# Kernel tuning notes

Hardware: AMD Instinct MI355X
Metric: run time of the kernel (lower is better)

Reference implementation:

```python
import jax, jax.numpy as jnp
import numpy as np

K = 2          # diffusion steps
HID = 64       # hidden_dim
T_OUT = 12     # decoder horizon
EPS = 1e-6


def _random_walk(A):
    # W_fwd = D_out^{-1} A ; W_bwd = D_in^{-1} A^T  (row-normalized)
    W_fwd = A / (A.sum(axis=1, keepdims=True) + EPS)
    AT = A.T
    W_bwd = AT / (AT.sum(axis=1, keepdims=True) + EPS)
    return W_fwd, W_bwd


def _dconv(xin, Wf, Wb, W, b):
    # xin: (B, N, F). K forward + K backward random-walk hops, concat, linear.
    outs = [xin]
    xf = xin
    for _ in range(K):
        xf = jnp.einsum('ij,bjf->bif', Wf, xf)
        outs.append(xf)
    xb = xin
    for _ in range(K):
        xb = jnp.einsum('ij,bjf->bif', Wb, xb)
        outs.append(xb)
    return jnp.concatenate(outs, axis=-1) @ W + b


def _cell(xl, h, Wr, br, Wz, bz, Wn, bn, Wf, Wb):
    xh = jnp.concatenate([xl, h], axis=-1)
    r = jax.nn.sigmoid(_dconv(xh, Wf, Wb, Wr, br))
    z = jax.nn.sigmoid(_dconv(xh, Wf, Wb, Wz, bz))
    xrh = jnp.concatenate([xl, r * h], axis=-1)
    n = jnp.tanh(_dconv(xrh, Wf, Wb, Wn, bn))
    return (1.0 - z) * h + z * n


def setup_inputs() -> dict:
    key = jax.random.key(0)
    ks = jax.random.split(key, 20)
    B, T_in, N = 16, 12, 512
    x = jax.random.normal(ks[0], (B, T_in, N), dtype=jnp.float32)
    A = jax.random.uniform(ks[1], (N, N), dtype=jnp.float32)

    def lin(k, fan_in, fan_out):
        s = 1.0 / np.sqrt(fan_in)
        kw, kb = jax.random.split(k)
        W = jax.random.uniform(kw, (fan_in, fan_out), jnp.float32, -s, s)
        b = jax.random.uniform(kb, (fan_out,), jnp.float32, -s, s)
        return W, b

    in0 = (2 * K + 1) * (1 + HID)    # 325
    in1 = (2 * K + 1) * (2 * HID)    # 640
    Wr0, br0 = lin(ks[2], in0, HID)
    Wz0, bz0 = lin(ks[3], in0, HID)
    Wn0, bn0 = lin(ks[4], in0, HID)
    Wr1, br1 = lin(ks[5], in1, HID)
    Wz1, bz1 = lin(ks[6], in1, HID)
    Wn1, bn1 = lin(ks[7], in1, HID)
    Wp, bp = lin(ks[8], HID, 1)
    return dict(x=x, A=A, Wr0=Wr0, br0=br0, Wz0=Wz0, bz0=bz0, Wn0=Wn0, bn0=bn0,
                Wr1=Wr1, br1=br1, Wz1=Wz1, bz1=bz1, Wn1=Wn1, bn1=bn1, Wp=Wp, bp=bp)


def reference(x, A, Wr0, br0, Wz0, bz0, Wn0, bn0,
              Wr1, br1, Wz1, bz1, Wn1, bn1, Wp, bp):
    Wf, Wb = _random_walk(A)
    B, T_in, N = x.shape
    x4 = x[..., None]                             # (B, T_in, N, 1)
    h0 = jnp.zeros((B, N, HID), x.dtype)
    h1 = jnp.zeros((B, N, HID), x.dtype)

    def enc_step(carry, xt):
        h0, h1 = carry
        h0 = _cell(xt, h0, Wr0, br0, Wz0, bz0, Wn0, bn0, Wf, Wb)
        h1 = _cell(h0, h1, Wr1, br1, Wz1, bz1, Wn1, bn1, Wf, Wb)
        return (h0, h1), None

    (h0, h1), _ = jax.lax.scan(enc_step, (h0, h1), jnp.moveaxis(x4, 1, 0))

    def dec_step(carry, _):
        h0, h1, di = carry
        h0 = _cell(di, h0, Wr0, br0, Wz0, bz0, Wn0, bn0, Wf, Wb)
        h1 = _cell(h0, h1, Wr1, br1, Wz1, bz1, Wn1, bn1, Wf, Wb)
        yt = h1 @ Wp + bp                          # (B, N, 1)
        return (h0, h1, yt), yt

    (_, _, _), ys = jax.lax.scan(dec_step, (h0, h1, x4[:, -1]), None, length=T_OUT)
    return jnp.moveaxis(ys, 0, 1)[..., 0]          # (B, T_out, N)
```

## Files before the change

### kernel.cpp

```cpp
#include <hip/hip_runtime.h>
#include <math.h>

#define T_IN   12
#define T_OUT  12
#define NB     8192
#define EPSV   1e-6f

typedef __attribute__((ext_vector_type(8))) short short8;
typedef __attribute__((ext_vector_type(4))) float floatx4;

__device__ __forceinline__ unsigned short f2bf(float x) {
    union { float f; unsigned u; } v; v.f = x;
    unsigned r = v.u + 0x7fffu + ((v.u >> 16) & 1u);
    return (unsigned short)(r >> 16);
}
__device__ __forceinline__ float bf2f(unsigned short h) {
    union { float f; unsigned u; } v; v.u = ((unsigned)h) << 16;
    return v.f;
}
__device__ __forceinline__ unsigned packbf(float v) {
    unsigned u = __float_as_uint(v);
    unsigned hu = u & 0xffff0000u;
    float r = v - __uint_as_float(hu);
    unsigned ru = __float_as_uint(r);
    return (ru & 0xffff0000u) | (u >> 16);
}
__device__ __forceinline__ void split2(float v, short& h, short& l) {
    unsigned u = __float_as_uint(v);
    h = (short)(u >> 16);
    float r = v - __uint_as_float(u & 0xffff0000u);
    l = (short)(__float_as_uint(r) >> 16);
}

__device__ __forceinline__ float sigmoid_fast(float x) {
    return 1.0f / (1.0f + __expf(-x));
}
__device__ __forceinline__ float tanh_fast(float x) {
    float e = __expf(2.0f * x);
    return 1.0f - 2.0f / (e + 1.0f);
}

struct HopA {
    const float* M[4];
    float* dst0[4];
};

struct HopM {
    const unsigned short* Ahi[4]; const unsigned short* Alo[4];
    const unsigned* src0; const unsigned* src1;
    unsigned* dst0[4]; unsigned* dst1[4];
    int tiles0;
};

struct XHopM {
    const unsigned short* Ahi[4]; const unsigned short* Alo[4];
    const float* X;
    float* Y;
    int ncols;
};

struct WPack { const float* w[4]; unsigned short* hi[4]; unsigned short* lo[4]; };

struct LPackAll { const float* W[6]; unsigned short* hi[6]; unsigned short* lo[6]; };

struct LinJob {
    const unsigned* seg[10]; int nseg;
    const float* sx[5]; int sxrow[5]; int nsx;
    const unsigned short* Wh[2]; const unsigned short* Wl[2];
    const float* WO[2]; const float* bias[2];
    const float* h; unsigned* GP; float* Z;
    float* PR;
    int mode;
};

struct NJob {
    const unsigned* seg[10]; int nseg; int ksplit;
    const float* sx[5]; int sxrow[5]; int nsx;
    const unsigned short* Wh; const unsigned short* Wl;
    const float* WO; const float* bias;
    const float* Zb; const float* hin; float* hout; unsigned* hPout;
    int doProj; const float* Wp; const float* bp; float* out; float* di; int t;
};

struct F0 {
    const float* M[4];
    const float* di;
    const float* PR;
    const float* WO[2]; const float* bias[2];
    const float* h0;
    unsigned* GP0; float* Z0; float* HXS;
};

__global__ void sumfill_kernel(const float* __restrict__ A, float* __restrict__ Wf,
                               float* __restrict__ Wb) {
    int i = blockIdx.x;
    int t = threadIdx.x;
    __shared__ float s1[256], s2[256];
    float a = A[i * 512 + t] + A[i * 512 + t + 256];
    float b = A[t * 512 + i] + A[(t + 256) * 512 + i];
    s1[t] = a; s2[t] = b;
    __syncthreads();
    for (int off = 128; off > 0; off >>= 1) {
        if (t < off) { s1[t] += s1[t + off]; s2[t] += s2[t + off]; }
        __syncthreads();
    }
    float irs = 1.0f / (s1[0] + EPSV);
    float ics = 1.0f / (s2[0] + EPSV);
    for (int j = t; j < 512; j += 256) {
        Wf[i * 512 + j] = A[i * 512 + j] * irs;
        Wb[i * 512 + j] = A[j * 512 + i] * ics;
    }
}

__global__ void xenc_kernel(const float* __restrict__ x, float* __restrict__ xenc) {
    int idx = blockIdx.x * 256 + threadIdx.x;
    if (idx >= T_IN * NB) return;
    int j = idx & 511;
    int b = (idx >> 9) & 15;
    int t = idx >> 13;
    xenc[t * NB + j * 16 + b] = x[(b * T_IN + t) * 512 + j];
}

__global__ __launch_bounds__(256) void ghop_kernel(HopA a) {
    int z = blockIdx.z;
    const float* Wm = a.M[z];
    const float* X = Wm;
    float* Y = a.dst0[z];
    int col0 = blockIdx.x * 64;
    int row0 = blockIdx.y * 64;
    int tid = threadIdx.x;
    int tx = tid & 15, ty = tid >> 4;
    int kkA = tid & 15, rrA = tid >> 4;
    int ccB = tid & 63, kkB = tid >> 6;

    __shared__ float As[16][68], Bs[16][68];
    float acc[4][4] = {};

    const float* wp = Wm + (row0 + rrA) * 512 + kkA;
    const float* xp = X + (size_t)(col0 + ccB) + (size_t)kkB * 512;

    float ra[4], rb[4];
#pragma unroll
    for (int p = 0; p < 4; ++p) ra[p] = wp[p * 16 * 512];
#pragma unroll
    for (int p = 0; p < 4; ++p) rb[p] = xp[(size_t)(p * 4) * 512];

    for (int k0 = 0; k0 < 512; k0 += 16) {
#pragma unroll
        for (int p = 0; p < 4; ++p) As[kkA][rrA + p * 16] = ra[p];
#pragma unroll
        for (int p = 0; p < 4; ++p) Bs[kkB + p * 4][ccB] = rb[p];
        __syncthreads();
        if (k0 + 16 < 512) {
            int kn = k0 + 16;
#pragma unroll
            for (int p = 0; p < 4; ++p) ra[p] = wp[p * 16 * 512 + kn];
#pragma unroll
            for (int p = 0; p < 4; ++p) rb[p] = xp[(size_t)(kn + p * 4) * 512];
        }
#pragma unroll
        for (int k = 0; k < 16; ++k) {
            const float4 a4 = *(const float4*)&As[k][ty * 4];
            const float4 b4 = *(const float4*)&Bs[k][tx * 4];
            float av[4] = { a4.x, a4.y, a4.z, a4.w };
            float bv[4] = { b4.x, b4.y, b4.z, b4.w };
#pragma unroll
            for (int i = 0; i < 4; ++i)
#pragma unroll
                for (int j = 0; j < 4; ++j)
                    acc[i][j] = fmaf(av[i], bv[j], acc[i][j]);
        }
        __syncthreads();
    }

    int colw = col0 + tx * 4;
#pragma unroll
    for (int i = 0; i < 4; ++i) {
        int row = row0 + ty * 4 + i;
        *(float4*)&Y[(size_t)row * 512 + colw] =
            make_float4(acc[i][0], acc[i][1], acc[i][2], acc[i][3]);
    }
}

__global__ void wpack_kernel(WPack a) {
    int z = blockIdx.y;
    int idx = blockIdx.x * 256 + threadIdx.x;
    int m = idx >> 9, k = idx & 511;
    float x = a.w[z][idx];
    unsigned short h = f2bf(x);
    unsigned short l = f2bf(x - bf2f(h));
    int p = (((m >> 4) * 64 + (k >> 3)) * 16 + (m & 15)) * 8 + (k & 7);
    a.hi[z][p] = h;
    a.lo[z][p] = l;
}

__global__ void lpack_all_kernel(LPackAll p) {
    int g = blockIdx.y;
    int nseg = (g < 3) ? 5 : 10;
    int idx = blockIdx.x * 256 + threadIdx.x;
    if (idx >= nseg * 4096) return;
    int j = idx & 7, ln = (idx >> 3) & 15, ntl = (idx >> 7) & 3, O = idx >> 9;
    int s = O >> 3, o8 = O & 7;
    int base = (g < 3) ? (65 * s + 1) : (64 * s);
    int row = base + o8 * 8 + j;
    int col = ntl * 16 + ln;
    float v = p.W[g][(size_t)row * 64 + col];
    unsigned short h = f2bf(v);
    p.hi[g][idx] = h;
    p.lo[g][idx] = f2bf(v - bf2f(h));
}

template<int MI>
__global__ __launch_bounds__(256) void hop_mfma(HopM a) {
    int z = blockIdx.z;
    int nt = blockIdx.x;
    const unsigned* X; unsigned* Y; int c0;
    if (nt < a.tiles0) { X = a.src0; Y = a.dst0[z]; c0 = nt * 64; }
    else { X = a.src1; Y = a.dst1[z]; c0 = (nt - a.tiles0) * 64; }
    const unsigned short* Ahi = a.Ahi[z];
    const unsigned short* Alo = a.Alo[z];
    int bm = blockIdx.y * (MI * 32);

    __shared__ unsigned short Bhi_s[2][64][40];
    __shared__ unsigned short Blo_s[2][64][40];

    int tid = threadIdx.x;
    int lane = tid & 63, w = tid >> 6;
    int wm = (w & 1) * (MI * 16), wn = (w >> 1) * 32;
    int ln = lane & 15, quad = lane >> 4;
    int sc = tid & 63, skh = tid >> 6;

    floatx4 acc[MI][2];
#pragma unroll
    for (int mi = 0; mi < MI; ++mi)
#pragma unroll
        for (int ci = 0; ci < 2; ++ci) acc[mi][ci] = (floatx4)0.0f;

    const unsigned* xbase = X + c0 + sc;
    int mtb = (bm + wm) >> 4;

    unsigned uv[8];
#pragma unroll
    for (int j = 0; j < 8; ++j)
        uv[j] = xbase[(size_t)(skh * 8 + j) * 1024];
    {
        short8 h8, l8;
#pragma unroll
        for (int j = 0; j < 8; ++j) {
            h8[j] = (short)(uv[j] & 0xffffu);
            l8[j] = (short)(uv[j] >> 16);
        }
        *(short8*)&Bhi_s[0][sc][skh * 8] = h8;
        *(short8*)&Blo_s[0][sc][skh * 8] = l8;
    }
#pragma unroll
    for (int j = 0; j < 8; ++j)
        uv[j] = xbase[(size_t)(32 + skh * 8 + j) * 1024];

    for (int it = 0; it < 16; ++it) {
        __syncthreads();
        int cur = it & 1;
        if (it + 1 < 16) {
            short8 h8, l8;
#pragma unroll
            for (int j = 0; j < 8; ++j) {
                h8[j] = (short)(uv[j] & 0xffffu);
                l8[j] = (short)(uv[j] >> 16);
            }
            *(short8*)&Bhi_s[cur ^ 1][sc][skh * 8] = h8;
            *(short8*)&Blo_s[cur ^ 1][sc][skh * 8] = l8;
        }
        if (it + 2 < 16) {
            int kn = (it + 2) * 32;
#pragma unroll
            for (int j = 0; j < 8; ++j)
                uv[j] = xbase[(size_t)(kn + skh * 8 + j) * 1024];
        }
        short8 bh[2], bl[2];
#pragma unroll
        for (int ci = 0; ci < 2; ++ci) {
            bh[ci] = *(const short8*)&Bhi_s[cur][wn + ci * 16 + ln][quad * 8];
            bl[ci] = *(const short8*)&Blo_s[cur][wn + ci * 16 + ln][quad * 8];
        }
        int kob = it * 4 + quad;
#pragma unroll
        for (int mi = 0; mi < MI; ++mi) {
            size_t aoff = ((size_t)((mtb + mi) * 64 + kob) * 16 + ln) * 8;
            short8 Ah = *(const short8*)(Ahi + aoff);
            short8 Al = *(const short8*)(Alo + aoff);
#pragma unroll
            for (int ci = 0; ci < 2; ++ci) {
                acc[mi][ci] = __builtin_amdgcn_mfma_f32_16x16x32_bf16(Ah, bh[ci], acc[mi][ci], 0, 0, 0);
                acc[mi][ci] = __builtin_amdgcn_mfma_f32_16x16x32_bf16(Ah, bl[ci], acc[mi][ci], 0, 0, 0);
                acc[mi][ci] = __builtin_amdgcn_mfma_f32_16x16x32_bf16(Al, bh[ci], acc[mi][ci], 0, 0, 0);
            }
        }
    }

#pragma unroll
    for (int mi = 0; mi < MI; ++mi) {
#pragma unroll
        for (int ci = 0; ci < 2; ++ci) {
            int mrow = bm + wm + mi * 16 + quad * 4;
            int col = c0 + wn + ci * 16 + ln;
#pragma unroll
            for (int r = 0; r < 4; ++r)
                Y[(size_t)(mrow + r) * 1024 + col] = packbf(acc[mi][ci][r]);
        }
    }
}

__global__ __launch_bounds__(256) void xhop_mfma(XHopM a) {
    int z = blockIdx.z;
    int c0 = blockIdx.x * 64;
    const unsigned short* Ahi = a.Ahi[z];
    const unsigned short* Alo = a.Alo[z];
    int bm = blockIdx.y * 64;

    __shared__ unsigned short Bhi_s[2][64][40];
    __shared__ unsigned short Blo_s[2][64][40];

    int tid = threadIdx.x;
    int lane = tid & 63, w = tid >> 6;
    int wm = (w & 1) * 32, wn = (w >> 1) * 32;
    int ln = lane & 15, quad = lane >> 4;
    int sc = tid & 63, skh = tid >> 6;

    floatx4 acc[2][2];
#pragma unroll
    for (int mi = 0; mi < 2; ++mi)
#pragma unroll
        for (int ci = 0; ci < 2; ++ci) acc[mi][ci] = (floatx4)0.0f;

    int colS = c0 + sc;
    bool ok = colS < a.ncols;
    const float* xb = a.X + (size_t)(colS >> 4) * NB + (colS & 15);
    int mtb = (bm + wm) >> 4;

    float xv[8];
#pragma unroll
    for (int j = 0; j < 8; ++j)
        xv[j] = ok ? xb[(size_t)(skh * 8 + j) * 16] : 0.0f;
    {
        short8 h8, l8;
#pragma unroll
        for (int j = 0; j < 8; ++j) { short h, l; split2(xv[j], h, l); h8[j] = h; l8[j] = l; }
        *(short8*)&Bhi_s[0][sc][skh * 8] = h8;
        *(short8*)&Blo_s[0][sc][skh * 8] = l8;
    }
#pragma unroll
    for (int j = 0; j < 8; ++j)
        xv[j] = ok ? xb[(size_t)(32 + skh * 8 + j) * 16] : 0.0f;

    for (int it = 0; it < 16; ++it) {
        __syncthreads();
        int cur = it & 1;
        if (it + 1 < 16) {
            short8 h8, l8;
#pragma unroll
            for (int j = 0; j < 8; ++j) { short h, l; split2(xv[j], h, l); h8[j] = h; l8[j] = l; }
            *(short8*)&Bhi_s[cur ^ 1][sc][skh * 8] = h8;
            *(short8*)&Blo_s[cur ^ 1][sc][skh * 8] = l8;
        }
        if (it + 2 < 16) {
            int kn = (it + 2) * 32;
#pragma unroll
            for (int j = 0; j < 8; ++j)
                xv[j] = ok ? xb[(size_t)(kn + skh * 8 + j) * 16] : 0.0f;
        }
        short8 bh[2], bl[2];
#pragma unroll
        for (int ci = 0; ci < 2; ++ci) {
            bh[ci] = *(const short8*)&Bhi_s[cur][wn + ci * 16 + ln][quad * 8];
            bl[ci] = *(const short8*)&Blo_s[cur][wn + ci * 16 + ln][quad * 8];
        }
        int kob = it * 4 + quad;
#pragma unroll
        for (int mi = 0; mi < 2; ++mi) {
            size_t aoff = ((size_t)((mtb + mi) * 64 + kob) * 16 + ln) * 8;
            short8 Ah = *(const short8*)(Ahi + aoff);
            short8 Al = *(const short8*)(Alo + aoff);
#pragma unroll
            for (int ci = 0; ci < 2; ++ci) {
                acc[mi][ci] = __builtin_amdgcn_mfma_f32_16x16x32_bf16(Ah, bh[ci], acc[mi][ci], 0, 0, 0);
                acc[mi][ci] = __builtin_amdgcn_mfma_f32_16x16x32_bf16(Ah, bl[ci], acc[mi][ci], 0, 0, 0);
                acc[mi][ci] = __builtin_amdgcn_mfma_f32_16x16x32_bf16(Al, bh[ci], acc[mi][ci], 0, 0, 0);
            }
        }
    }

#pragma unroll
    for (int mi = 0; mi < 2; ++mi) {
#pragma unroll
        for (int ci = 0; ci < 2; ++ci) {
            int col = c0 + wn + ci * 16 + ln;
            if (col < a.ncols) {
                int mrow = bm + wm + mi * 16 + quad * 4;
                float* yb = a.Y + (size_t)((col >> 4) * 4 + z) * NB + (col & 15);
#pragma unroll
                for (int r = 0; r < 4; ++r)
                    yb[(size_t)(mrow + r) * 16] = acc[mi][ci][r];
            }
        }
    }
}

__device__ __forceinline__ void lin_core2(const unsigned* const* segs, int nseg, int s0,
        const unsigned short* __restrict__ Bh, const unsigned short* __restrict__ Bl,
        int row0, int ln, int quad, int cihalf, floatx4 acc[2]) {
    for (int s = 0; s < nseg; ++s) {
        const unsigned* ap = segs[s] + (size_t)(row0 + ln) * 64 + quad * 8;
#pragma unroll
        for (int hh = 0; hh < 2; ++hh) {
            unsigned u[8];
            *(uint4*)&u[0] = *(const uint4*)(ap + hh * 32);
            *(uint4*)&u[4] = *(const uint4*)(ap + hh * 32 + 4);
            short8 Ah, Al;
#pragma unroll
            for (int j = 0; j < 8; ++j) {
                Ah[j] = (short)(u[j] & 0xffffu);
                Al[j] = (short)(u[j] >> 16);
            }
            int O = (s0 + s) * 8 + hh * 4 + quad;
#pragma unroll
            for (int ci = 0; ci < 2; ++ci) {
                int c_abs = cihalf * 2 + ci;
                size_t boff = ((size_t)(O * 4 + c_abs) * 16 + ln) * 8;
                short8 B1 = *(const short8*)(Bh + boff);
                short8 B2 = *(const short8*)(Bl + boff);
                acc[ci] = __builtin_amdgcn_mfma_f32_16x16x32_bf16(Ah, B1, acc[ci], 0, 0, 0);
                acc[ci] = __builtin_amdgcn_mfma_f32_16x16x32_bf16(Al, B1, acc[ci], 0, 0, 0);
                acc[ci] = __builtin_amdgcn_mfma_f32_16x16x32_bf16(Ah, B2, acc[ci], 0, 0, 0);
            }
        }
    }
}

__device__ __forceinline__ void lin_scalar2p(const float* const* sx, const int* sxrow,
        int nsx, const float* __restrict__ WO,
        int row0, int ln, int quad, int cihalf, floatx4 acc[2]) {
    for (int t = 0; t < nsx; ++t) {
        const float* wr = WO + (size_t)sxrow[t] * 64;
        const float* sv = sx[t] + row0 + quad * 4;
#pragma unroll
        for (int rr = 0; rr < 4; ++rr) {
            float v = sv[rr];
#pragma unroll
            for (int ci = 0; ci < 2; ++ci)
                acc[ci][rr] = fmaf(v, wr[(cihalf * 2 + ci) * 16 + ln], acc[ci][rr]);
        }
    }
}

__device__ __forceinline__ void rz_body(const LinJob& J, int bx) {
    int w = threadIdx.x >> 6, lane = threadIdx.x & 63;
    int ln = lane & 15, quad = lane >> 4;
    int row0 = bx * 64 + w * 16;
    int gate = blockIdx.y;
    int cihalf = blockIdx.z;
    floatx4 acc[2];
    acc[0] = (floatx4)0.0f; acc[1] = (floatx4)0.0f;
    lin_core2(J.seg, J.nseg, 0, J.Wh[gate], J.Wl[gate], row0, ln, quad, cihalf, acc);
    if (J.nsx) lin_scalar2p(J.sx, J.sxrow, J.nsx, J.WO[gate], row0, ln, quad, cihalf, acc);
    if (J.mode == 0) {
        const float* bias = J.bias[gate];
#pragma unroll
        for (int ci = 0; ci < 2; ++ci) {
            int col = (cihalf * 2 + ci) * 16 + ln;
            float bv = bias[col];
#pragma unroll
            for (int rr = 0; rr < 4; ++rr) {
                int row = row0 + quad * 4 + rr;
                size_t idx = (size_t)row * 64 + col;
                float sg = sigmoid_fast(acc[ci][rr] + bv);
                if (gate == 0) J.GP[idx] = packbf(sg * J.h[idx]);
                else J.Z[idx] = sg;
            }
        }
    } else {
        float* PRg = J.PR + (size_t)gate * ((size_t)NB * 64);
#pragma unroll
        for (int ci = 0; ci < 2; ++ci) {
            int col = (cihalf * 2 + ci) * 16 + ln;
#pragma unroll
            for (int rr = 0; rr < 4; ++rr) {
                int row = row0 + quad * 4 + rr;
                PRg[(size_t)row * 64 + col] = acc[ci][rr];
            }
        }
    }
}

__global__ __launch_bounds__(256) void lin_rz2(LinJob j0, LinJob j1, int xsplit) {
    if ((int)blockIdx.x >= xsplit) rz_body(j1, (int)blockIdx.x - xsplit);
    else                           rz_body(j0, (int)blockIdx.x);
}

__device__ __forceinline__ void n_body(const NJob& J, int bx) {
    int w = threadIdx.x >> 6, lane = threadIdx.x & 63;
    int ln = lane & 15, quad = lane >> 4;
    int kh = w & 1, cihalf = w >> 1;
    int row0 = bx * 16;
    __shared__ float part[2][2][16][17];
    __shared__ float pr[2][16];
    floatx4 acc[2];
    acc[0] = (floatx4)0.0f; acc[1] = (floatx4)0.0f;
    if (kh == 0) {
        lin_core2(J.seg, J.ksplit, 0, J.Wh, J.Wl, row0, ln, quad, cihalf, acc);
    } else {
        lin_core2(J.seg + J.ksplit, J.nseg - J.ksplit, J.ksplit, J.Wh, J.Wl,
                  row0, ln, quad, cihalf, acc);
        if (J.nsx) lin_scalar2p(J.sx, J.sxrow, J.nsx, J.WO, row0, ln, quad, cihalf, acc);
#pragma unroll
        for (int ci = 0; ci < 2; ++ci)
#pragma unroll
            for (int rr = 0; rr < 4; ++rr)
                part[cihalf][ci][quad * 4 + rr][ln] = acc[ci][rr];
    }
    __syncthreads();
    float p[4] = {0.0f, 0.0f, 0.0f, 0.0f};
    if (kh == 0) {
#pragma unroll
        for (int ci = 0; ci < 2; ++ci) {
            int col = (cihalf * 2 + ci) * 16 + ln;
            float bv = J.bias[col];
            float wpv = J.doProj ? J.Wp[col] : 0.0f;
#pragma unroll
            for (int rr = 0; rr < 4; ++rr) {
                int row = row0 + quad * 4 + rr;
                size_t idx = (size_t)row * 64 + col;
                float pre = acc[ci][rr] + part[cihalf][ci][quad * 4 + rr][ln] + bv;
                float nn = tanh_fast(pre);
                float z = J.Zb[idx];
                float hv = J.hin[idx];
                float o = (1.0f - z) * hv + z * nn;
                J.hout[idx] = o;
                J.hPout[idx] = packbf(o);
                p[rr] = fmaf(o, wpv, p[rr]);
            }
        }
        if (J.doProj) {
#pragma unroll
            for (int rr = 0; rr < 4; ++rr) {
                p[rr] += __shfl_xor(p[rr], 1, 64);
                p[rr] += __shfl_xor(p[rr], 2, 64);
                p[rr] += __shfl_xor(p[rr], 4, 64);
                p[rr] += __shfl_xor(p[rr], 8, 64);
            }
            if (ln == 0) {
#pragma unroll
                for (int rr = 0; rr < 4; ++rr)
                    pr[cihalf][quad * 4 + rr] = p[rr];
            }
        }
    }
    __syncthreads();
    if (J.doProj && kh == 0 && cihalf == 0 && ln == 0) {
        float bpv = J.bp[0];
#pragma unroll
        for (int rr = 0; rr < 4; ++rr) {
            int qr = quad * 4 + rr;
            int row = row0 + qr;
            float y = pr[0][qr] + pr[1][qr] + bpv;
            int n = row >> 4, b = row & 15;
            J.out[(b * T_OUT + J.t) * 512 + n] = y;
            J.di[row] = y;
        }
    }
}

__global__ __launch_bounds__(256) void lin_n2(NJob j0, NJob j1, int xsplit) {
    if ((int)blockIdx.x >= xsplit) n_body(j1, (int)blockIdx.x - xsplit);
    else                           n_body(j0, (int)blockIdx.x);
}

__global__ __launch_bounds__(256) void finish0_kernel(F0 a) {
    int n = blockIdx.x;
    int tid = threadIdx.x;
    __shared__ float hopS[4][16];
    __shared__ float sdi[16];

    int g = tid >> 2;
    int sub = tid & 3;
    int m = g >> 4, b = g & 15;
    const float* wrow = a.M[m] + (size_t)n * 512 + sub * 128;
    const float* dv = a.di + (size_t)(sub * 128) * 16 + b;
    float s0 = 0.0f, s1 = 0.0f, s2 = 0.0f, s3 = 0.0f;
#pragma unroll 8
    for (int k = 0; k < 128; k += 4) {
        float4 w4 = *(const float4*)&wrow[k];
        s0 = fmaf(w4.x, dv[(k + 0) * 16], s0);
        s1 = fmaf(w4.y, dv[(k + 1) * 16], s1);
        s2 = fmaf(w4.z, dv[(k + 2) * 16], s2);
        s3 = fmaf(w4.w, dv[(k + 3) * 16], s3);
    }
    float sv = (s0 + s1) + (s2 + s3);
    sv += __shfl_xor(sv, 1, 64);
    sv += __shfl_xor(sv, 2, 64);
    if (sub == 0) {
        hopS[m][b] = sv;
        a.HXS[(size_t)m * NB + n * 16 + b] = sv;
    }
    if (tid < 16) sdi[tid] = a.di[n * 16 + tid];
    __syncthreads();

    int gate = tid >> 7, col = tid & 63, rh = (tid >> 6) & 1;
    const float* WOg = a.WO[gate];
    float w0c = WOg[col];
    float wmc[4];
#pragma unroll
    for (int mm = 0; mm < 4; ++mm)
        wmc[mm] = WOg[(size_t)(65 * (mm + 1)) * 64 + col];
    float bv = a.bias[gate][col];
    const float* PRg = a.PR + (size_t)gate * ((size_t)NB * 64);
#pragma unroll
    for (int rr = 0; rr < 8; ++rr) {
        int bl = rh * 8 + rr;
        int row = n * 16 + bl;
        size_t idx = (size_t)row * 64 + col;
        float pre = PRg[idx] + bv + sdi[bl] * w0c;
#pragma unroll
        for (int mm = 0; mm < 4; ++mm)
            pre = fmaf(hopS[mm][bl], wmc[mm], pre);
        float sg = sigmoid_fast(pre);
        if (gate == 0) a.GP0[idx] = packbf(sg * a.h0[idx]);
        else a.Z0[idx] = sg;
    }
}

extern "C" void kernel_launch(void* const* d_in, const int* in_sizes, int n_in,
                              void* d_out, int out_size, void* d_ws, size_t ws_size,
                              hipStream_t stream) {
    (void)in_sizes; (void)n_in; (void)out_size; (void)ws_size;
    const float* x   = (const float*)d_in[0];
    const float* A   = (const float*)d_in[1];
    const float* Wr0 = (const float*)d_in[2];  const float* br0 = (const float*)d_in[3];
    const float* Wz0 = (const float*)d_in[4];  const float* bz0 = (const float*)d_in[5];
    const float* Wn0 = (const float*)d_in[6];  const float* bn0 = (const float*)d_in[7];
    const float* Wr1 = (const float*)d_in[8];  const float* br1 = (const float*)d_in[9];
    const float* Wz1 = (const float*)d_in[10]; const float* bz1 = (const float*)d_in[11];
    const float* Wn1 = (const float*)d_in[12]; const float* bn1 = (const float*)d_in[13];
    const float* Wp  = (const float*)d_in[14]; const float* bp  = (const float*)d_in[15];
    float* out = (float*)d_out;

    float* ws = (float*)d_ws;
    size_t off = 0;
    auto alloc = [&](size_t nf) { float* p = ws + off; off += nf; return p; };
    const size_t NB64 = (size_t)NB * 64;
    float* Wf  = alloc(262144); float* Wb  = alloc(262144);
    float* W2f = alloc(262144); float* W2b = alloc(262144);
    float* xenc = alloc((size_t)T_IN * NB);
    unsigned short* Whi[4]; unsigned short* Wlo[4];
    for (int m = 0; m < 4; ++m) Whi[m] = (unsigned short*)alloc(131072);
    for (int m = 0; m < 4; ++m) Wlo[m] = (unsigned short*)alloc(131072);
    float* zbase = alloc(12 * NB64);
    float* h0x[2]; unsigned* h0Px[2];
    h0x[1]  = zbase;
    h0Px[1] = (unsigned*)(zbase + NB64);
    float* h1 = zbase + 2 * NB64;
    unsigned* h1P = (unsigned*)(zbase + 3 * NB64);
    unsigned* HAall = (unsigned*)(zbase + 4 * NB64);
    unsigned* HBall = (unsigned*)(zbase + 8 * NB64);
    unsigned* HA[4]; unsigned* HB[4]; unsigned* HG0[4]; unsigned* HG1[4];
    for (int m = 0; m < 4; ++m) HA[m] = HAall + m * NB64;
    for (int m = 0; m < 4; ++m) HB[m] = HBall + m * NB64;
    for (int m = 0; m < 4; ++m) HG0[m] = (unsigned*)alloc(NB64);
    for (int m = 0; m < 4; ++m) HG1[m] = (unsigned*)alloc(NB64);
    unsigned* GP0 = (unsigned*)alloc(NB64);
    unsigned* GP1 = (unsigned*)alloc(NB64);
    float* Z0 = alloc(NB64);
    float* Z1 = alloc(NB64);
    h0x[0]  = alloc(NB64);
    h0Px[0] = (unsigned*)alloc(NB64);
    float* PR0 = alloc(2 * NB64);
    float* XHE = alloc((size_t)T_IN * 4 * NB);
    float* HXSdec = alloc(4 * NB);
    float* di = alloc(NB);
    unsigned short* LWh[6]; unsigned short* LWl[6];
    for (int g = 0; g < 3; ++g) { LWh[g] = (unsigned short*)alloc(10240); LWl[g] = (unsigned short*)alloc(10240); }
    for (int g = 3; g < 6; ++g) { LWh[g] = (unsigned short*)alloc(20480); LWl[g] = (unsigned short*)alloc(20480); }

    hipMemsetAsync(zbase, 0, 12 * NB64 * 4, stream);

    xenc_kernel<<<dim3((T_IN * NB) / 256), 256, 0, stream>>>(x, xenc);
    sumfill_kernel<<<dim3(512), 256, 0, stream>>>(A, Wf, Wb);
    {
        HopA w2 = {};
        w2.M[0] = Wf; w2.M[1] = Wb;
        w2.dst0[0] = W2f; w2.dst0[1] = W2b;
        ghop_kernel<<<dim3(8, 8, 2), 256, 0, stream>>>(w2);
    }
    {
        WPack p;
        p.w[0] = Wf; p.w[1] = W2f; p.w[2] = Wb; p.w[3] = W2b;
        for (int m = 0; m < 4; ++m) { p.hi[m] = Whi[m]; p.lo[m] = Wlo[m]; }
        wpack_kernel<<<dim3(1024, 4), 256, 0, stream>>>(p);
    }
    {
        LPackAll p;
        const float* WG[6] = { Wr0, Wz0, Wn0, Wr1, Wz1, Wn1 };
        for (int g = 0; g < 6; ++g) { p.W[g] = WG[g]; p.hi[g] = LWh[g]; p.lo[g] = LWl[g]; }
        lpack_all_kernel<<<dim3(160, 6), 256, 0, stream>>>(p);
    }
    {
        XHopM xa = {};
        for (int m = 0; m < 4; ++m) { xa.Ahi[m] = Whi[m]; xa.Alo[m] = Wlo[m]; }
        xa.X = xenc; xa.Y = XHE; xa.ncols = 192;
        xhop_mfma<<<dim3(3, 8, 4), 256, 0, stream>>>(xa);
    }

    auto hopSingle = [&](const unsigned* s0, unsigned* const* d0) {
        HopM a = {};
        for (int m = 0; m < 4; ++m) { a.Ahi[m] = Whi[m]; a.Alo[m] = Wlo[m]; }
        a.src0 = s0; a.tiles0 = 16;
        for (int m = 0; m < 4; ++m) a.dst0[m] = d0[m];
        hop_mfma<1><<<dim3(16, 16, 4), 256, 0, stream>>>(a);
    };
    auto hopDual = [&](const unsigned* s0, unsigned* const* d0,
                       const unsigned* s1, unsigned* const* d1) {
        HopM a = {};
        for (int m = 0; m < 4; ++m) { a.Ahi[m] = Whi[m]; a.Alo[m] = Wlo[m]; }
        a.src0 = s0; a.tiles0 = 16;
        for (int m = 0; m < 4; ++m) a.dst0[m] = d0[m];
        a.src1 = s1;
        for (int m = 0; m < 4; ++m) a.dst1[m] = d1[m];
        hop_mfma<2><<<dim3(32, 8, 4), 256, 0, stream>>>(a);
    };

    auto mkRZ1 = [&](int t) {
        LinJob J = {};
        J.seg[0] = h0Px[t & 1]; J.seg[1] = h1P;
        for (int m = 0; m < 4; ++m) { J.seg[2 + 2 * m] = HA[m]; J.seg[3 + 2 * m] = HB[m]; }
        J.nseg = 10; J.nsx = 0;
        J.Wh[0] = LWh[3]; J.Wl[0] = LWl[3]; J.Wh[1] = LWh[4]; J.Wl[1] = LWl[4];
        J.WO[0] = Wr1; J.WO[1] = Wz1; J.bias[0] = br1; J.bias[1] = bz1;
        J.h = h1; J.GP = GP1; J.Z = Z1; J.mode = 0;
        return J;
    };
    auto mkRZ0 = [&](int tn, const float* xc, const float* hx, int mode) {
        LinJob J = {};
        J.seg[0] = h0Px[(tn - 1) & 1];
        for (int m = 0; m < 4; ++m) J.seg[1 + m] = HA[m];
        J.nseg = 5;
        if (mode == 0) {
            J.nsx = 5;
            J.sx[0] = xc; J.sxrow[0] = 0;
            for (int m = 0; m < 4; ++m) { J.sx[1 + m] = hx + (size_t)m * NB; J.sxrow[1 + m] = 65 * (m + 1); }
        }
        J.Wh[0] = LWh[0]; J.Wl[0] = LWl[0]; J.Wh[1] = LWh[1]; J.Wl[1] = LWl[1];
        J.WO[0] = Wr0; J.WO[1] = Wz0; J.bias[0] = br0; J.bias[1] = bz0;
        J.h = h0x[(tn - 1) & 1]; J.GP = GP0; J.Z = Z0; J.PR = PR0; J.mode = mode;
        return J;
    };
    auto mkN1 = [&](int t) {
        NJob J = {};
        J.seg[0] = h0Px[t & 1]; J.seg[1] = GP1;
        for (int m = 0; m < 4; ++m) { J.seg[2 + 2 * m] = HA[m]; J.seg[3 + 2 * m] = HG1[m]; }
        J.nseg = 10; J.ksplit = 5; J.nsx = 0;
        J.Wh = LWh[5]; J.Wl = LWl[5]; J.WO = Wn1; J.bias = bn1;
        J.Zb = Z1; J.hin = h1; J.hout = h1; J.hPout = h1P;
        J.doProj = (t >= T_IN); J.Wp = Wp; J.bp = bp; J.out = out; J.di = di; J.t = t - T_IN;
        return J;
    };
    auto mkN0 = [&](int tn, const float* xc, const float* hx) {
        NJob J = {};
        J.seg[0] = GP0;
        for (int m = 0; m < 4; ++m) J.seg[1 + m] = HG0[m];
        J.nseg = 5; J.ksplit = 3;
        J.nsx = 5;
        J.sx[0] = xc; J.sxrow[0] = 0;
        for (int m = 0; m < 4; ++m) { J.sx[1 + m] = hx + (size_t)m * NB; J.sxrow[1 + m] = 65 * (m + 1); }
        J.Wh = LWh[2]; J.Wl = LWl[2]; J.WO = Wn0; J.bias = bn0;
        J.Zb = Z0; J.hin = h0x[(tn - 1) & 1]; J.hout = h0x[tn & 1]; J.hPout = h0Px[tn & 1];
        J.doProj = 0;
        return J;
    };

    auto rz2one = [&](LinJob a) { lin_rz2<<<dim3(128, 2, 2), 256, 0, stream>>>(a, a, 128); };
    auto rz2two = [&](LinJob a, LinJob b) { lin_rz2<<<dim3(256, 2, 2), 256, 0, stream>>>(a, b, 128); };
    auto n2one = [&](NJob a) { lin_n2<<<dim3(512), 256, 0, stream>>>(a, a, 512); };
    auto n2two = [&](NJob a, NJob b) { lin_n2<<<dim3(1024), 256, 0, stream>>>(a, b, 512); };

    rz2one(mkRZ0(0, xenc, XHE, 0));
    hopSingle(GP0, HG0);
    n2one(mkN0(0, xenc, XHE));
    hopSingle(h0Px[0], HA);

    for (int t = 0; t < T_IN + T_OUT; ++t) {
        int tn = t + 1;
        bool last = (t == T_IN + T_OUT - 1);
        bool decFeed = (tn >= T_IN + 1);
        if (!last && !decFeed) {
            int ts = (tn < T_IN) ? tn : (T_IN - 1);
            const float* xc = xenc + (size_t)ts * NB;
            const float* hx = XHE + (size_t)ts * 4 * NB;
            rz2two(mkRZ1(t), mkRZ0(tn, xc, hx, 0));
            hopDual(GP1, HG1, GP0, HG0);
            n2two(mkN1(t), mkN0(tn, xc, hx));
            hopDual(h0Px[tn & 1], HA, h1P, HB);
        } else if (!last) {
            rz2two(mkRZ1(t), mkRZ0(tn, nullptr, nullptr, 1));
            hopSingle(GP1, HG1);
            n2one(mkN1(t));
            {
                F0 f = {};
                f.M[0] = Wf; f.M[1] = W2f; f.M[2] = Wb; f.M[3] = W2b;
                f.di = di; f.PR = PR0;
                f.WO[0] = Wr0; f.WO[1] = Wz0; f.bias[0] = br0; f.bias[1] = bz0;
                f.h0 = h0x[t & 1];
                f.GP0 = GP0; f.Z0 = Z0; f.HXS = HXSdec;
                finish0_kernel<<<dim3(512), 256, 0, stream>>>(f);
            }
            hopSingle(GP0, HG0);
            n2one(mkN0(tn, di, HXSdec));
            hopDual(h0Px[tn & 1], HA, h1P, HB);
        } else {
            rz2one(mkRZ1(t));
            hopSingle(GP1, HG1);
            n2one(mkN1(t));
        }
    }
}
```

Before: 2.712 ms.

## Share B operand across two hop matrices per block and drop LDS staging

The hop kernel now computes two of the four random-walk matrix products per block, so each loaded activation tile feeds both matrices' MFMAs. It also removes the double-buffered shared-memory staging and __syncthreads, loading B fragments straight from global memory into registers. The goal is to halve redundant activation loads and cut synchronisation overhead. The cost is uncoalesced strided global loads per lane with no LDS reuse across waves, plus more register pressure.

```diff
diff --git a/kernel.cpp b/kernel.cpp
--- a/kernel.cpp
+++ b/kernel.cpp
@@ -210,102 +210,78 @@
     p.lo[g][idx] = f2bf(v - bf2f(h));
 }
 
-template<int MI>
-__global__ __launch_bounds__(256) void hop_mfma(HopM a) {
-    int z = blockIdx.z;
+__global__ __launch_bounds__(256) void hop2_mfma(HopM a) {
+    int zp = blockIdx.z;
     int nt = blockIdx.x;
-    const unsigned* X; unsigned* Y; int c0;
-    if (nt < a.tiles0) { X = a.src0; Y = a.dst0[z]; c0 = nt * 64; }
-    else { X = a.src1; Y = a.dst1[z]; c0 = (nt - a.tiles0) * 64; }
-    const unsigned short* Ahi = a.Ahi[z];
-    const unsigned short* Alo = a.Alo[z];
-    int bm = blockIdx.y * (MI * 32);
-
-    __shared__ unsigned short Bhi_s[2][64][40];
-    __shared__ unsigned short Blo_s[2][64][40];
+    const unsigned* X; unsigned* Y0; unsigned* Y1; int c0;
+    if (nt < a.tiles0) {
+        X = a.src0; Y0 = a.dst0[2 * zp]; Y1 = a.dst0[2 * zp + 1]; c0 = nt * 64;
+    } else {
+        X = a.src1; Y0 = a.dst1[2 * zp]; Y1 = a.dst1[2 * zp + 1];
+        c0 = (nt - a.tiles0) * 64;
+    }
+    const unsigned short* Ahi0 = a.Ahi[2 * zp];
+    const unsigned short* Alo0 = a.Alo[2 * zp];
+    const unsigned short* Ahi1 = a.Ahi[2 * zp + 1];
+    const unsigned short* Alo1 = a.Alo[2 * zp + 1];
+    int bm = blockIdx.y * 32;
 
     int tid = threadIdx.x;
     int lane = tid & 63, w = tid >> 6;
-    int wm = (w & 1) * (MI * 16), wn = (w >> 1) * 32;
+    int wm = (w & 1) * 16, wn = (w >> 1) * 32;
     int ln = lane & 15, quad = lane >> 4;
-    int sc = tid & 63, skh = tid >> 6;
-
-    floatx4 acc[MI][2];
-#pragma unroll
-    for (int mi = 0; mi < MI; ++mi)
-#pragma unroll
-        for (int ci = 0; ci < 2; ++ci) acc[mi][ci] = (floatx4)0.0f;
-
-    const unsigned* xbase = X + c0 + sc;
     int mtb = (bm + wm) >> 4;
 
-    unsigned uv[8];
-#pragma unroll
-    for (int j = 0; j < 8; ++j)
-        uv[j] = xbase[(size_t)(skh * 8 + j) * 1024];
-    {
-        short8 h8, l8;
-#pragma unroll
-        for (int j = 0; j < 8; ++j) {
-            h8[j] = (short)(uv[j] & 0xffffu);
-            l8[j] = (short)(uv[j] >> 16);
-        }
-        *(short8*)&Bhi_s[0][sc][skh * 8] = h8;
-        *(short8*)&Blo_s[0][sc][skh * 8] = l8;
-    }
-#pragma unroll
-    for (int j = 0; j < 8; ++j)
-        uv[j] = xbase[(size_t)(32 + skh * 8 + j) * 1024];
-
+    floatx4 acc[2][2];
+#pragma unroll
+    for (int zz = 0; zz < 2; ++zz)
+#pragma unroll
+        for (int ci = 0; ci < 2; ++ci) acc[zz][ci] = (floatx4)0.0f;
+
+    const unsigned* xc = X + c0 + wn + ln;
+
+#pragma unroll
     for (int it = 0; it < 16; ++it) {
-        __syncthreads();
-        int cur = it & 1;
-        if (it + 1 < 16) {
-            short8 h8, l8;
+        int kob = it * 4 + quad;
+        const unsigned* base = xc + (size_t)(kob * 8) * 1024;
+        unsigned u[2][8];
+#pragma unroll
+        for (int ci = 0; ci < 2; ++ci)
+#pragma unroll
+            for (int j = 0; j < 8; ++j)
+                u[ci][j] = base[ci * 16 + (size_t)j * 1024];
+        size_t aoff = ((size_t)(mtb * 64 + kob) * 16 + ln) * 8;
+        short8 A0h = *(const short8*)(Ahi0 + aoff);
+        short8 A0l = *(const short8*)(Alo0 + aoff);
+        short8 A1h = *(const short8*)(Ahi1 + aoff);
+        short8 A1l = *(const short8*)(Alo1 + aoff);
+#pragma unroll
+        for (int ci = 0; ci < 2; ++ci) {
+            short8 bh, bl;
 #pragma unroll
             for (int j = 0; j < 8; ++j) {
-                h8[j] = (short)(uv[j] & 0xffffu);
-                l8[j] = (short)(uv[j] >> 16);
-            }
-            *(short8*)&Bhi_s[cur ^ 1][sc][skh * 8] = h8;
-            *(short8*)&Blo_s[cur ^ 1][sc][skh * 8] = l8;
-        }
-        if (it + 2 < 16) {
-            int kn = (it + 2) * 32;
-#pragma unroll
-            for (int j = 0; j < 8; ++j)
-                uv[j] = xbase[(size_t)(kn + skh * 8 + j) * 1024];
-        }
-        short8 bh[2], bl[2];
+                bh[j] = (short)(u[ci][j] & 0xffffu);
+                bl[j] = (short)(u[ci][j] >> 16);
+            }
+            acc[0][ci] = __builtin_amdgcn_mfma_f32_16x16x32_bf16(A0h, bh, acc[0][ci], 0, 0, 0);
+            acc[0][ci] = __builtin_amdgcn_mfma_f32_16x16x32_bf16(A0h, bl, acc[0][ci], 0, 0, 0);
+            acc[0][ci] = __builtin_amdgcn_mfma_f32_16x16x32_bf16(A0l, bh, acc[0][ci], 0, 0, 0);
+            acc[1][ci] = __builtin_amdgcn_mfma_f32_16x16x32_bf16(A1h, bh, acc[1][ci], 0, 0, 0);
+            acc[1][ci] = __builtin_amdgcn_mfma_f32_16x16x32_bf16(A1h, bl, acc[1][ci], 0, 0, 0);
+            acc[1][ci] = __builtin_amdgcn_mfma_f32_16x16x32_bf16(A1l, bh, acc[1][ci], 0, 0, 0);
+        }
+    }
+
+#pragma unroll
+    for (int zz = 0; zz < 2; ++zz) {
+        unsigned* Y = zz ? Y1 : Y0;
 #pragma unroll
         for (int ci = 0; ci < 2; ++ci) {
-            bh[ci] = *(const short8*)&Bhi_s[cur][wn + ci * 16 + ln][quad * 8];
-            bl[ci] = *(const short8*)&Blo_s[cur][wn + ci * 16 + ln][quad * 8];
-        }
-        int kob = it * 4 + quad;
-#pragma unroll
-        for (int mi = 0; mi < MI; ++mi) {
-            size_t aoff = ((size_t)((mtb + mi) * 64 + kob) * 16 + ln) * 8;
-            short8 Ah = *(const short8*)(Ahi + aoff);
-            short8 Al = *(const short8*)(Alo + aoff);
-#pragma unroll
-            for (int ci = 0; ci < 2; ++ci) {
-                acc[mi][ci] = __builtin_amdgcn_mfma_f32_16x16x32_bf16(Ah, bh[ci], acc[mi][ci], 0, 0, 0);
-                acc[mi][ci] = __builtin_amdgcn_mfma_f32_16x16x32_bf16(Ah, bl[ci], acc[mi][ci], 0, 0, 0);
-                acc[mi][ci] = __builtin_amdgcn_mfma_f32_16x16x32_bf16(Al, bh[ci], acc[mi][ci], 0, 0, 0);
-            }
-        }
-    }
-
-#pragma unroll
-    for (int mi = 0; mi < MI; ++mi) {
-#pragma unroll
-        for (int ci = 0; ci < 2; ++ci) {
-            int mrow = bm + wm + mi * 16 + quad * 4;
+            int mrow = bm + wm + quad * 4;
             int col = c0 + wn + ci * 16 + ln;
 #pragma unroll
             for (int r = 0; r < 4; ++r)
-                Y[(size_t)(mrow + r) * 1024 + col] = packbf(acc[mi][ci][r]);
+                Y[(size_t)(mrow + r) * 1024 + col] = packbf(acc[zz][ci][r]);
         }
     }
 }
@@ -714,7 +690,7 @@
         for (int m = 0; m < 4; ++m) { a.Ahi[m] = Whi[m]; a.Alo[m] = Wlo[m]; }
         a.src0 = s0; a.tiles0 = 16;
         for (int m = 0; m < 4; ++m) a.dst0[m] = d0[m];
-        hop_mfma<1><<<dim3(16, 16, 4), 256, 0, stream>>>(a);
+        hop2_mfma<<<dim3(16, 16, 2), 256, 0, stream>>>(a);
     };
     auto hopDual = [&](const unsigned* s0, unsigned* const* d0,
                        const unsigned* s1, unsigned* const* d1) {
@@ -724,7 +700,7 @@
         for (int m = 0; m < 4; ++m) a.dst0[m] = d0[m];
         a.src1 = s1;
         for (int m = 0; m < 4; ++m) a.dst1[m] = d1[m];
-        hop_mfma<2><<<dim3(32, 8, 4), 256, 0, stream>>>(a);
+        hop2_mfma<<<dim3(32, 16, 2), 256, 0, stream>>>(a);
     };
 
     auto mkRZ1 = [&](int t) {
```

After: 2.933 ms. 1.08x slower.
